# Kernel tuning notes

Measured on AMD Instinct MI355X. Metric: run time of the kernel, lower is better.

The kernel has to match this reference:

```python
import jax, jax.numpy as jnp
import numpy as np

N_NODES = 100000
N_EDGES = 3200000
INPUT_DIM = 128
HIDDEN = 64


def spmm(row, col, vals, x, n):
    # out[i] = sum_{e: row[e]==i} vals[e] * x[col[e]]  -- COO SpMM via gather + segment_sum
    msgs = vals[:, None] * x[col]  # [E, F]
    return jax.ops.segment_sum(msgs, row, num_segments=n)


def setup_inputs() -> dict:
    key = jax.random.key(0)
    ks = jax.random.split(key, 12)
    embeddings = jax.random.normal(ks[0], (N_NODES, INPUT_DIM), dtype=jnp.float32)
    norm_degrees = jax.random.uniform(ks[1], (N_NODES, 1), dtype=jnp.float32)
    seed_mask = (jax.random.uniform(ks[2], (N_NODES, 1)) < 0.05).astype(jnp.float32)
    adj_row = jax.random.randint(ks[3], (N_EDGES,), 0, N_NODES, dtype=jnp.int32)
    adj_col = jax.random.randint(ks[4], (N_EDGES,), 0, N_NODES, dtype=jnp.int32)
    adj_vals = jax.random.uniform(ks[5], (N_EDGES,), dtype=jnp.float32)
    d_in = INPUT_DIM + 2
    # Linear params (torch Linear: y = x @ W.T + b); store W as [in, out]
    W1 = jax.random.normal(ks[6], (d_in, HIDDEN), dtype=jnp.float32) / np.sqrt(d_in)
    b1 = jnp.zeros((HIDDEN,), dtype=jnp.float32)
    W2 = jax.random.normal(ks[7], (HIDDEN, HIDDEN), dtype=jnp.float32) / np.sqrt(HIDDEN)
    b2 = jnp.zeros((HIDDEN,), dtype=jnp.float32)
    W_out = jax.random.normal(ks[8], (HIDDEN, 1), dtype=jnp.float32) / np.sqrt(HIDDEN)
    b_out = jnp.zeros((1,), dtype=jnp.float32)
    return {
        "embeddings": embeddings, "norm_degrees": norm_degrees, "seed_mask": seed_mask,
        "adj_row": adj_row, "adj_col": adj_col, "adj_vals": adj_vals,
        "W1": W1, "b1": b1, "W2": W2, "b2": b2, "W_out": W_out, "b_out": b_out,
    }


def reference(embeddings, norm_degrees, seed_mask, adj_row, adj_col, adj_vals,
              W1, b1, W2, b2, W_out, b_out):
    n = embeddings.shape[0]
    x = jnp.concatenate([embeddings, norm_degrees, seed_mask], axis=1)  # [N, input_dim+2]
    x = x @ W1 + b1                       # conv1
    x = jax.nn.relu(spmm(adj_row, adj_col, adj_vals, x, n))
    x = x @ W2 + b2                       # conv2
    x = jax.nn.relu(spmm(adj_row, adj_col, adj_vals, x, n))
    graph_rep = jnp.sum(x, axis=0)        # [HIDDEN]
    return graph_rep @ W_out + b_out      # [1]
```

## Files before the change

### kernel.cpp

```cpp
#include <hip/hip_runtime.h>
#include <hip/hip_bf16.h>

#define HID 64
#define IN_EMB 128
#define IN_DIM 130
#define ROWS_PER_BKT 512
#define LOG_RPB 9
#define MAX_BKT 256
#define PART_CHUNK 8192
#define SLOT_E 18432
#define ASTR 168
#define BSTR 72
#define ECAP 1024

typedef __hip_bfloat16 bf16;
typedef __attribute__((ext_vector_type(8))) short bf16x8;
typedef __attribute__((ext_vector_type(4))) float fx4;
typedef __attribute__((ext_vector_type(2))) float fx2;

__device__ __forceinline__ short f2bfs(float f) {
  __hip_bfloat16 h = __float2bfloat16(f);
  return *(reinterpret_cast<short*>(&h));
}
__device__ __forceinline__ int pk_fp8x4(float a, float b, float c, float d) {
  int v = __builtin_amdgcn_cvt_pk_fp8_f32(a, b, 0, false);
  v = __builtin_amdgcn_cvt_pk_fp8_f32(c, d, v, true);
  return v;
}
__device__ __forceinline__ unsigned char f2fp8(float x) {
  return (unsigned char)(__builtin_amdgcn_cvt_pk_fp8_f32(x, x, 0, false) & 0xFF);
}

__global__ __launch_bounds__(1024) void bscan_kernel(const int* __restrict__ bcnt,
                                                     int* __restrict__ bstart,
                                                     int* __restrict__ row_ptr,
                                                     int n, int nbkt) {
  __shared__ int s[1024];
  const int t = threadIdx.x;
  const int v = (t < nbkt) ? bcnt[t] : 0;
  s[t] = v;
  __syncthreads();
  for (int off = 1; off < 1024; off <<= 1) {
    int u = (t >= off) ? s[t - off] : 0;
    __syncthreads();
    s[t] += u;
    __syncthreads();
  }
  if (t < nbkt) bstart[t] = s[t] - v;
  if (t == 0) { bstart[nbkt] = s[1023]; row_ptr[n] = s[1023]; }
}

__global__ __launch_bounds__(512) void partition_kernel(
    const int* __restrict__ row, const int* __restrict__ col,
    const float* __restrict__ vals, int* __restrict__ bcur,
    int2* __restrict__ tmp, int nE) {
  __shared__ int h[MAX_BKT];
  __shared__ int cur[MAX_BKT];
  const int t = threadIdx.x;
  const int base = blockIdx.x * PART_CHUNK;
  for (int i = t; i < MAX_BKT; i += 512) h[i] = 0;
  __syncthreads();
  for (int kk = t; kk < PART_CHUNK / 4; kk += 512) {
    int e0 = base + kk * 4;
    if (e0 + 3 < nE) {
      int4 r4 = ((const int4*)row)[(base >> 2) + kk];
      atomicAdd(&h[r4.x >> LOG_RPB], 1);
      atomicAdd(&h[r4.y >> LOG_RPB], 1);
      atomicAdd(&h[r4.z >> LOG_RPB], 1);
      atomicAdd(&h[r4.w >> LOG_RPB], 1);
    } else {
      for (int j = 0; j < 4; ++j) {
        int e = e0 + j;
        if (e < nE) atomicAdd(&h[row[e] >> LOG_RPB], 1);
      }
    }
  }
  __syncthreads();
  for (int b = t; b < MAX_BKT; b += 512)
    if (h[b] > 0) cur[b] = b * SLOT_E + atomicAdd(&bcur[b], h[b]);
  __syncthreads();
  for (int kk = t; kk < PART_CHUNK / 4; kk += 512) {
    int e0 = base + kk * 4;
    if (e0 + 3 < nE) {
      int4 r4 = ((const int4*)row)[(base >> 2) + kk];
      int4 c4 = ((const int4*)col)[(base >> 2) + kk];
      float4 v4 = ((const float4*)vals)[(base >> 2) + kk];
      int rr[4] = {r4.x, r4.y, r4.z, r4.w};
      int cc[4] = {c4.x, c4.y, c4.z, c4.w};
      float vv[4] = {v4.x, v4.y, v4.z, v4.w};
#pragma unroll
      for (int j = 0; j < 4; ++j) {
        int b = rr[j] >> LOG_RPB;
        int p = atomicAdd(&cur[b], 1);
        if (p - b * SLOT_E < SLOT_E)
          tmp[p] = make_int2(cc[j] | ((rr[j] & (ROWS_PER_BKT - 1)) << 20),
                             __float_as_int(vv[j]));
      }
    } else {
      for (int j = 0; j < 4; ++j) {
        int e = e0 + j;
        if (e < nE) {
          int r = row[e];
          int b = r >> LOG_RPB;
          int p = atomicAdd(&cur[b], 1);
          if (p - b * SLOT_E < SLOT_E)
            tmp[p] = make_int2(col[e] | ((r & (ROWS_PER_BKT - 1)) << 20),
                               __float_as_int(vals[e]));
        }
      }
    }
  }
}

__global__ __launch_bounds__(512) void bucket_sort_kernel(
    const int* __restrict__ bstart, const int2* __restrict__ tmp,
    int2* __restrict__ ce, int* __restrict__ row_ptr, int n) {
  __shared__ int rcnt[ROWS_PER_BKT];
  __shared__ int rpos[ROWS_PER_BKT];
  __shared__ int sc[ROWS_PER_BKT];
  const int t = threadIdx.x;
  const int b = blockIdx.x;
  const int start = bstart[b];
  const int len   = bstart[b + 1] - start;
  const int2* ts = tmp + (size_t)b * SLOT_E;
  rcnt[t] = 0;
  __syncthreads();
  const int* keys = (const int*)ts;
  for (int i = t; i < len; i += 512)
    atomicAdd(&rcnt[((unsigned)keys[2 * i]) >> 20], 1);
  __syncthreads();
  sc[t] = rcnt[t];
  __syncthreads();
  for (int off = 1; off < ROWS_PER_BKT; off <<= 1) {
    int u = (t >= off) ? sc[t - off] : 0;
    __syncthreads();
    sc[t] += u;
    __syncthreads();
  }
  {
    int ex = sc[t] - rcnt[t];
    int gpos = start + ex;
    rpos[t] = gpos;
    int gr = b * ROWS_PER_BKT + t;
    if (gr < n) row_ptr[gr] = gpos;
  }
  __syncthreads();
  for (int i = t; i < len; i += 512) {
    int2 e = ts[i];
    int p = atomicAdd(&rpos[((unsigned)e.x) >> 20], 1);
    ce[p] = make_int2(e.x & 0xFFFFF, e.y);
  }
}

__global__ __launch_bounds__(256) void lin1_kernel(
    const float* __restrict__ emb, const float* __restrict__ deg,
    const float* __restrict__ seed, const float* __restrict__ W1,
    const float* __restrict__ b1, unsigned char* __restrict__ out, int n) {
  __shared__ short sB[64 * ASTR];
  const int t = threadIdx.x;
  const int base = blockIdx.x * 256;

  for (int idx = t; idx < 64 * 160; idx += 256) {
    int k = idx >> 6, nn = idx & 63;
    float v = (k < IN_DIM) ? W1[k * HID + nn] : 0.f;
    sB[nn * ASTR + k] = f2bfs(v);
  }
  __syncthreads();

  const int lane = t & 63, w = t >> 6;
  const int nl = lane & 15, q = lane >> 4;
  const short* pB = &sB[nl * ASTR + q * 8];
  const float bias0 = b1[nl], bias1 = b1[16 + nl],
              bias2 = b1[32 + nl], bias3 = b1[48 + nl];

#pragma unroll
  for (int tile = 0; tile < 4; ++tile) {
    const int g64 = base + tile * 64;
    const int anode = g64 + w * 16 + nl;
    bf16x8 afr[5];
    if (anode < n) {
      const float4* ep = (const float4*)(emb + (size_t)anode * IN_EMB);
#pragma unroll
      for (int kt = 0; kt < 4; ++kt) {
        float4 v0 = ep[q * 2 + kt * 8];
        float4 v1 = ep[q * 2 + 1 + kt * 8];
        bf16x8 a;
        a[0] = f2bfs(v0.x); a[1] = f2bfs(v0.y); a[2] = f2bfs(v0.z); a[3] = f2bfs(v0.w);
        a[4] = f2bfs(v1.x); a[5] = f2bfs(v1.y); a[6] = f2bfs(v1.z); a[7] = f2bfs(v1.w);
        afr[kt] = a;
      }
      bf16x8 a4 = {0, 0, 0, 0, 0, 0, 0, 0};
      if (q == 0) { a4[0] = f2bfs(deg[anode]); a4[1] = f2bfs(seed[anode]); }
      afr[4] = a4;
    } else {
#pragma unroll
      for (int kt = 0; kt < 5; ++kt) afr[kt] = (bf16x8){0, 0, 0, 0, 0, 0, 0, 0};
    }

    fx4 ac0 = {0.f, 0.f, 0.f, 0.f}, ac1 = ac0, ac2 = ac0, ac3 = ac0;
#pragma unroll
    for (int kt = 0; kt < 5; ++kt) {
      bf16x8 b0  = *(const bf16x8*)(pB + kt * 32);
      bf16x8 b1v = *(const bf16x8*)(pB + 16 * ASTR + kt * 32);
      bf16x8 b2v = *(const bf16x8*)(pB + 32 * ASTR + kt * 32);
      bf16x8 b3v = *(const bf16x8*)(pB + 48 * ASTR + kt * 32);
      ac0 = __builtin_amdgcn_mfma_f32_16x16x32_bf16(afr[kt], b0,  ac0, 0, 0, 0);
      ac1 = __builtin_amdgcn_mfma_f32_16x16x32_bf16(afr[kt], b1v, ac1, 0, 0, 0);
      ac2 = __builtin_amdgcn_mfma_f32_16x16x32_bf16(afr[kt], b2v, ac2, 0, 0, 0);
      ac3 = __builtin_amdgcn_mfma_f32_16x16x32_bf16(afr[kt], b3v, ac3, 0, 0, 0);
    }
#pragma unroll
    for (int r = 0; r < 4; ++r) {
      int node = g64 + w * 16 + q * 4 + r;
      if (node < n) {
        unsigned char* o = out + ((size_t)node << 6);
        o[nl]      = f2fp8(ac0[r] + bias0);
        o[16 + nl] = f2fp8(ac1[r] + bias1);
        o[32 + nl] = f2fp8(ac2[r] + bias2);
        o[48 + nl] = f2fp8(ac3[r] + bias3);
      }
    }
  }
}

#define GLD(ev, u)                                                            \
  const uint2 u = *(const uint2*)(xp + (((size_t)(unsigned)(ev)) << 6) + 8 * fl);
#define GMAD(ev, u)                                                           \
  {                                                                           \
    const float v = __int_as_float((int)((ev) >> 32));                        \
    const fx2 v2 = {v, v};                                                    \
    a0 += v2 * __builtin_amdgcn_cvt_pk_f32_fp8(u.x, false);                   \
    a1 += v2 * __builtin_amdgcn_cvt_pk_f32_fp8(u.x, true);                    \
    a2 += v2 * __builtin_amdgcn_cvt_pk_f32_fp8(u.y, false);                   \
    a3 += v2 * __builtin_amdgcn_cvt_pk_f32_fp8(u.y, true);                    \
  }
#define GMAD_P(ev, u, ok)                                                     \
  {                                                                           \
    const float v = (ok) ? __int_as_float((int)((ev) >> 32)) : 0.f;           \
    const fx2 v2 = {v, v};                                                    \
    a0 += v2 * __builtin_amdgcn_cvt_pk_f32_fp8(u.x, false);                   \
    a1 += v2 * __builtin_amdgcn_cvt_pk_f32_fp8(u.x, true);                    \
    a2 += v2 * __builtin_amdgcn_cvt_pk_f32_fp8(u.y, false);                   \
    a3 += v2 * __builtin_amdgcn_cvt_pk_f32_fp8(u.y, true);                    \
  }

#define SPMM_STAGE_EDGES                                                      \
  const unsigned long long* cep = (const unsigned long long*)ce;              \
  const int r0blk = blockIdx.x * 4;                                           \
  const int bstartE = row_ptr[r0blk];                                         \
  const int bendE = row_ptr[(r0blk + 4 < n) ? (r0blk + 4) : n];               \
  const int cnt = min(bendE - bstartE, ECAP);                                 \
  for (int ii = threadIdx.x; ii < cnt; ii += 256)                             \
    eb[ii] = __builtin_nontemporal_load(cep + bstartE + ii);                  \
  __syncthreads();

#define SPMM_GATHER_BODY                                                      \
  const int i0r = row_ptr[r];                                                 \
  const int endr = row_ptr[r + 1];                                            \
  int li = i0r - bstartE;                                                     \
  const int lend = endr - bstartE;                                            \
  if (lend <= cnt) {                                                          \
    for (; li + 32 <= lend; li += 32) {                                       \
      unsigned long long e0 = eb[li + sub];                                   \
      unsigned long long e1 = eb[li + 8 + sub];                               \
      unsigned long long e2 = eb[li + 16 + sub];                              \
      unsigned long long e3 = eb[li + 24 + sub];                              \
      GLD(e0, u0); GLD(e1, u1); GLD(e2, u2); GLD(e3, u3);                     \
      GMAD(e0, u0); GMAD(e1, u1); GMAD(e2, u2); GMAD(e3, u3);                 \
    }                                                                         \
    if (li < lend) {                                                          \
      const int last = lend - 1;                                              \
      int i0 = li + sub;        bool k0 = i0 < lend;                          \
      int i1 = li + 8 + sub;    bool k1 = i1 < lend;                          \
      int i2 = li + 16 + sub;   bool k2 = i2 < lend;                          \
      int i3 = li + 24 + sub;   bool k3 = i3 < lend;                          \
      unsigned long long e0 = eb[k0 ? i0 : last];                             \
      unsigned long long e1 = eb[k1 ? i1 : last];                             \
      unsigned long long e2 = eb[k2 ? i2 : last];                             \
      unsigned long long e3 = eb[k3 ? i3 : last];                             \
      GLD(e0, u0); GLD(e1, u1); GLD(e2, u2); GLD(e3, u3);                     \
      GMAD_P(e0, u0, k0); GMAD_P(e1, u1, k1);                                 \
      GMAD_P(e2, u2, k2); GMAD_P(e3, u3, k3);                                 \
    }                                                                         \
  } else {                                                                    \
    int i = i0r;                                                              \
    for (; i + 32 <= endr; i += 32) {                                         \
      unsigned long long e0 = __builtin_nontemporal_load(cep + i + sub);      \
      unsigned long long e1 = __builtin_nontemporal_load(cep + i + 8 + sub);  \
      unsigned long long e2 = __builtin_nontemporal_load(cep + i + 16 + sub); \
      unsigned long long e3 = __builtin_nontemporal_load(cep + i + 24 + sub); \
      GLD(e0, u0); GLD(e1, u1); GLD(e2, u2); GLD(e3, u3);                     \
      GMAD(e0, u0); GMAD(e1, u1); GMAD(e2, u2); GMAD(e3, u3);                 \
    }                                                                         \
    if (i < endr) {                                                           \
      const int last = endr - 1;                                              \
      int i0 = i + sub;        bool k0 = i0 < endr;                           \
      int i1 = i + 8 + sub;    bool k1 = i1 < endr;                           \
      int i2 = i + 16 + sub;   bool k2 = i2 < endr;                           \
      int i3 = i + 24 + sub;   bool k3 = i3 < endr;                           \
      unsigned long long e0 = cep[k0 ? i0 : last];                            \
      unsigned long long e1 = cep[k1 ? i1 : last];                            \
      unsigned long long e2 = cep[k2 ? i2 : last];                            \
      unsigned long long e3 = cep[k3 ? i3 : last];                            \
      GLD(e0, u0); GLD(e1, u1); GLD(e2, u2); GLD(e3, u3);                     \
      GMAD_P(e0, u0, k0); GMAD_P(e1, u1, k1);                                 \
      GMAD_P(e2, u2, k2); GMAD_P(e3, u3, k3);                                 \
    }                                                                         \
  }                                                                           \
                      \
  _Pragma("unroll")                                                           \
  for (int off = 8; off <= 32; off <<= 1) {                                   \
    a0.x += __shfl_xor(a0.x, off); a0.y += __shfl_xor(a0.y, off);             \
    a1.x += __shfl_xor(a1.x, off); a1.y += __shfl_xor(a1.y, off);             \
    a2.x += __shfl_xor(a2.x, off); a2.y += __shfl_xor(a2.y, off);             \
    a3.x += __shfl_xor(a3.x, off); a3.y += __shfl_xor(a3.y, off);             \
  }

__global__ __launch_bounds__(256) void spmm_csr_kernel(
    const int* __restrict__ row_ptr, const int2* __restrict__ ce,
    const unsigned char* __restrict__ x, unsigned char* __restrict__ y, int n) {
  __shared__ unsigned long long eb[ECAP];
  const int lane = threadIdx.x & 63;
  const int sub = lane >> 3;
  const int fl  = lane & 7;
  const int r = blockIdx.x * 4 + (threadIdx.x >> 6);
  const unsigned char* xp = x;
  SPMM_STAGE_EDGES
  if (r < n) {
    fx2 a0 = {0.f, 0.f}, a1 = a0, a2 = a0, a3 = a0;
    SPMM_GATHER_BODY
    if (sub == 0) {
      int lo = pk_fp8x4(fmaxf(a0.x, 0.f), fmaxf(a0.y, 0.f),
                        fmaxf(a1.x, 0.f), fmaxf(a1.y, 0.f));
      int hi = pk_fp8x4(fmaxf(a2.x, 0.f), fmaxf(a2.y, 0.f),
                        fmaxf(a3.x, 0.f), fmaxf(a3.y, 0.f));
      *(int2*)(y + ((size_t)r << 6) + 8 * fl) = make_int2(lo, hi);
    }
  }
}

__global__ __launch_bounds__(256) void lin2_kernel(
    const unsigned char* __restrict__ yin, const float* __restrict__ W2,
    const float* __restrict__ b2, unsigned char* __restrict__ xout, int n) {
  __shared__ short sB[64 * BSTR];
  const int t = threadIdx.x;
  const int base = blockIdx.x * 256;
  for (int idx = t; idx < 64 * 64; idx += 256) {
    int k = idx >> 6, nn = idx & 63;
    sB[nn * BSTR + k] = f2bfs(W2[k * HID + nn]);
  }
  __syncthreads();

  const int lane = t & 63, w = t >> 6;
  const int nl = lane & 15, q = lane >> 4;
  const short* pB = &sB[nl * BSTR + q * 8];
  const float bias0 = b2[nl], bias1 = b2[16 + nl],
              bias2 = b2[32 + nl], bias3 = b2[48 + nl];

#pragma unroll
  for (int tile = 0; tile < 4; ++tile) {
    const int g64 = base + tile * 64;
    const int anode = g64 + w * 16 + nl;
    const unsigned char* xg = yin + (((size_t)anode) << 6) + q * 8;
    fx4 ac0 = {0.f, 0.f, 0.f, 0.f}, ac1 = ac0, ac2 = ac0, ac3 = ac0;
#pragma unroll
    for (int kt = 0; kt < 2; ++kt) {
      uint2 u8 = (anode < n) ? *(const uint2*)(xg + kt * 32) : make_uint2(0u, 0u);
      fx2 f0 = __builtin_amdgcn_cvt_pk_f32_fp8(u8.x, false);
      fx2 f1 = __builtin_amdgcn_cvt_pk_f32_fp8(u8.x, true);
      fx2 f2 = __builtin_amdgcn_cvt_pk_f32_fp8(u8.y, false);
      fx2 f3 = __builtin_amdgcn_cvt_pk_f32_fp8(u8.y, true);
      bf16x8 a;
      a[0] = f2bfs(f0.x); a[1] = f2bfs(f0.y); a[2] = f2bfs(f1.x); a[3] = f2bfs(f1.y);
      a[4] = f2bfs(f2.x); a[5] = f2bfs(f2.y); a[6] = f2bfs(f3.x); a[7] = f2bfs(f3.y);
      bf16x8 b0  = *(const bf16x8*)(pB + kt * 32);
      bf16x8 b1v = *(const bf16x8*)(pB + 16 * BSTR + kt * 32);
      bf16x8 b2v = *(const bf16x8*)(pB + 32 * BSTR + kt * 32);
      bf16x8 b3v = *(const bf16x8*)(pB + 48 * BSTR + kt * 32);
      ac0 = __builtin_amdgcn_mfma_f32_16x16x32_bf16(a, b0,  ac0, 0, 0, 0);
      ac1 = __builtin_amdgcn_mfma_f32_16x16x32_bf16(a, b1v, ac1, 0, 0, 0);
      ac2 = __builtin_amdgcn_mfma_f32_16x16x32_bf16(a, b2v, ac2, 0, 0, 0);
      ac3 = __builtin_amdgcn_mfma_f32_16x16x32_bf16(a, b3v, ac3, 0, 0, 0);
    }
#pragma unroll
    for (int r = 0; r < 4; ++r) {
      int node = g64 + w * 16 + q * 4 + r;
      if (node < n) {
        unsigned char* o = xout + ((size_t)node << 6);
        o[nl]      = f2fp8(ac0[r] + bias0);
        o[16 + nl] = f2fp8(ac1[r] + bias1);
        o[32 + nl] = f2fp8(ac2[r] + bias2);
        o[48 + nl] = f2fp8(ac3[r] + bias3);
      }
    }
  }
}

__global__ __launch_bounds__(256) void spmm2_fused_kernel(
    const int* __restrict__ row_ptr, const int2* __restrict__ ce,
    const unsigned char* __restrict__ x, const float* __restrict__ Wout,
    float* __restrict__ partials, int n) {
  __shared__ unsigned long long eb[ECAP];
  const int lane = threadIdx.x & 63;
  const int sub = lane >> 3;
  const int fl  = lane & 7;
  const int g = threadIdx.x >> 6;
  const int r = blockIdx.x * 4 + g;
  const unsigned char* xp = x;
  SPMM_STAGE_EDGES
  float wpart = 0.f;
  if (r < n) {
    fx2 a0 = {0.f, 0.f}, a1 = a0, a2 = a0, a3 = a0;
    SPMM_GATHER_BODY
    if (sub == 0) {
      const float4 wv0 = ((const float4*)Wout)[2 * fl];
      const float4 wv1 = ((const float4*)Wout)[2 * fl + 1];
      wpart = fmaxf(a0.x, 0.f) * wv0.x + fmaxf(a0.y, 0.f) * wv0.y
            + fmaxf(a1.x, 0.f) * wv0.z + fmaxf(a1.y, 0.f) * wv0.w
            + fmaxf(a2.x, 0.f) * wv1.x + fmaxf(a2.y, 0.f) * wv1.y
            + fmaxf(a3.x, 0.f) * wv1.z + fmaxf(a3.y, 0.f) * wv1.w;
    }
  }
  for (int off = 32; off; off >>= 1) wpart += __shfl_down(wpart, off, 64);
  __shared__ float part[4];
  if (lane == 0) part[g] = wpart;
  __syncthreads();
  if (threadIdx.x == 0)
    partials[blockIdx.x] = part[0] + part[1] + part[2] + part[3];
}

__global__ __launch_bounds__(1024) void reduce_kernel(
    const float* __restrict__ partials, const float* __restrict__ bout,
    float* __restrict__ out, int m) {
  const int t = threadIdx.x;
  float s = 0.f;
  const int m4 = m >> 2;
  for (int i = t; i < m4; i += 1024) {
    float4 v = ((const float4*)partials)[i];
    s += v.x + v.y + v.z + v.w;
  }
  if (t < (m & 3)) s += partials[(m & ~3) + t];
  for (int off = 32; off; off >>= 1) s += __shfl_down(s, off, 64);
  __shared__ float wsum[16];
  if ((t & 63) == 0) wsum[t >> 6] = s;
  __syncthreads();
  if (t == 0) {
    float tot = bout[0];
    for (int w = 0; w < 16; ++w) tot += wsum[w];
    out[0] = tot;
  }
}

extern "C" void kernel_launch(void* const* d_in, const int* in_sizes, int n_in,
                              void* d_out, int out_size, void* d_ws, size_t ws_size,
                              hipStream_t stream) {
  const float* emb  = (const float*)d_in[0];
  const float* deg  = (const float*)d_in[1];
  const float* seed = (const float*)d_in[2];
  const int*   row  = (const int*)d_in[3];
  const int*   col  = (const int*)d_in[4];
  const float* vals = (const float*)d_in[5];
  const float* W1   = (const float*)d_in[6];
  const float* b1   = (const float*)d_in[7];
  const float* W2   = (const float*)d_in[8];
  const float* b2   = (const float*)d_in[9];
  const float* Wout = (const float*)d_in[10];
  const float* bout = (const float*)d_in[11];
  float* out = (float*)d_out;

  const int n  = in_sizes[0] / IN_EMB;
  const int nE = in_sizes[3];
  const int nbkt = (n + ROWS_PER_BKT - 1) / ROWS_PER_BKT;

  const int lin_blocks  = (n + 255) / 256;
  const int row_blocks  = (n + 3) / 4;
  const int part_blocks = (nE + PART_CHUNK - 1) / PART_CHUNK;

  char* ws = (char*)d_ws;
  int2* ce   = (int2*)ws;  ws += (size_t)nE * sizeof(int2);
  char* tmpb = ws;
  int2* tmp  = (int2*)ws;  ws += (size_t)nbkt * SLOT_E * sizeof(int2);
  unsigned char* xb = (unsigned char*)ws;  ws += ((size_t)n * HID + 255) & ~255ULL;
  int* row_ptr = (int*)ws; ws += ((size_t)(n + 1) * 4 + 255) & ~255ULL;
  int* bcur    = (int*)ws; ws += ((size_t)nbkt * 4 + 255) & ~255ULL;
  int* bstart  = (int*)ws; ws += ((size_t)(nbkt + 1) * 4 + 255) & ~255ULL;
  float* partials = (float*)ws;
  unsigned char* xa = (unsigned char*)tmpb;
  unsigned char* ya = (unsigned char*)(tmpb + (8u << 20));

  hipMemsetAsync(bcur, 0, (size_t)nbkt * sizeof(int), stream);
  partition_kernel<<<part_blocks, 512, 0, stream>>>(row, col, vals, bcur, tmp, nE);
  bscan_kernel<<<1, 1024, 0, stream>>>(bcur, bstart, row_ptr, n, nbkt);
  bucket_sort_kernel<<<nbkt, 512, 0, stream>>>(bstart, tmp, ce, row_ptr, n);

  lin1_kernel<<<lin_blocks, 256, 0, stream>>>(emb, deg, seed, W1, b1, xa, n);
  spmm_csr_kernel<<<row_blocks, 256, 0, stream>>>(row_ptr, ce, xa, ya, n);
  lin2_kernel<<<lin_blocks, 256, 0, stream>>>(ya, W2, b2, xb, n);
  spmm2_fused_kernel<<<row_blocks, 256, 0, stream>>>(row_ptr, ce, xb, Wout, partials, n);
  reduce_kernel<<<1, 1024, 0, stream>>>(partials, bout, out, row_blocks);
}
```

Before: 331.5 us.

## Map each SpMM row to 8 lanes instead of a full wavefront

The CSR SpMM kernels now assign one row per group of 8 lanes, 32 rows per 256-thread block, rather than one row per 64-lane wavefront. Each lane walks the row's edges sequentially in steps of 4, which removes the cross-lane shuffle reduction and leaves no lanes idle in the output stage. The shared-memory edge staging buffer is doubled to cover 32 rows' edges. The cost is less memory-level parallelism per row and more lane divergence between rows of different degree, plus higher LDS use per block.

```diff
diff --git a/kernel.cpp b/kernel.cpp
--- a/kernel.cpp
+++ b/kernel.cpp
@@ -11,7 +11,8 @@
 #define SLOT_E 18432
 #define ASTR 168
 #define BSTR 72
-#define ECAP 1024
+#define RPB 32
+#define ECAP 2048
 
 typedef __hip_bfloat16 bf16;
 typedef __attribute__((ext_vector_type(8))) short bf16x8;
@@ -246,9 +247,9 @@
 
 #define SPMM_STAGE_EDGES                                                      \
   const unsigned long long* cep = (const unsigned long long*)ce;              \
-  const int r0blk = blockIdx.x * 4;                                           \
+  const int r0blk = blockIdx.x * RPB;                                         \
   const int bstartE = row_ptr[r0blk];                                         \
-  const int bendE = row_ptr[(r0blk + 4 < n) ? (r0blk + 4) : n];               \
+  const int bendE = row_ptr[(r0blk + RPB < n) ? (r0blk + RPB) : n];           \
   const int cnt = min(bendE - bstartE, ECAP);                                 \
   for (int ii = threadIdx.x; ii < cnt; ii += 256)                             \
     eb[ii] = __builtin_nontemporal_load(cep + bstartE + ii);                  \
@@ -257,85 +258,67 @@
 #define SPMM_GATHER_BODY                                                      \
   const int i0r = row_ptr[r];                                                 \
   const int endr = row_ptr[r + 1];                                            \
-  int li = i0r - bstartE;                                                     \
   const int lend = endr - bstartE;                                            \
   if (lend <= cnt) {                                                          \
-    for (; li + 32 <= lend; li += 32) {                                       \
-      unsigned long long e0 = eb[li + sub];                                   \
-      unsigned long long e1 = eb[li + 8 + sub];                               \
-      unsigned long long e2 = eb[li + 16 + sub];                              \
-      unsigned long long e3 = eb[li + 24 + sub];                              \
+    int i = i0r - bstartE;                                                    \
+    for (; i + 4 <= lend; i += 4) {                                           \
+      unsigned long long e0 = eb[i];                                          \
+      unsigned long long e1 = eb[i + 1];                                      \
+      unsigned long long e2 = eb[i + 2];                                      \
+      unsigned long long e3 = eb[i + 3];                                      \
       GLD(e0, u0); GLD(e1, u1); GLD(e2, u2); GLD(e3, u3);                     \
       GMAD(e0, u0); GMAD(e1, u1); GMAD(e2, u2); GMAD(e3, u3);                 \
     }                                                                         \
-    if (li < lend) {                                                          \
+    if (i < lend) {                                                           \
       const int last = lend - 1;                                              \
-      int i0 = li + sub;        bool k0 = i0 < lend;                          \
-      int i1 = li + 8 + sub;    bool k1 = i1 < lend;                          \
-      int i2 = li + 16 + sub;   bool k2 = i2 < lend;                          \
-      int i3 = li + 24 + sub;   bool k3 = i3 < lend;                          \
-      unsigned long long e0 = eb[k0 ? i0 : last];                             \
-      unsigned long long e1 = eb[k1 ? i1 : last];                             \
-      unsigned long long e2 = eb[k2 ? i2 : last];                             \
-      unsigned long long e3 = eb[k3 ? i3 : last];                             \
+      bool k1 = i + 1 < lend, k2 = i + 2 < lend, k3 = i + 3 < lend;           \
+      unsigned long long e0 = eb[i];                                          \
+      unsigned long long e1 = eb[k1 ? i + 1 : last];                          \
+      unsigned long long e2 = eb[k2 ? i + 2 : last];                          \
+      unsigned long long e3 = eb[k3 ? i + 3 : last];                          \
       GLD(e0, u0); GLD(e1, u1); GLD(e2, u2); GLD(e3, u3);                     \
-      GMAD_P(e0, u0, k0); GMAD_P(e1, u1, k1);                                 \
+      GMAD(e0, u0); GMAD_P(e1, u1, k1);                                       \
       GMAD_P(e2, u2, k2); GMAD_P(e3, u3, k3);                                 \
     }                                                                         \
   } else {                                                                    \
     int i = i0r;                                                              \
-    for (; i + 32 <= endr; i += 32) {                                         \
-      unsigned long long e0 = __builtin_nontemporal_load(cep + i + sub);      \
-      unsigned long long e1 = __builtin_nontemporal_load(cep + i + 8 + sub);  \
-      unsigned long long e2 = __builtin_nontemporal_load(cep + i + 16 + sub); \
-      unsigned long long e3 = __builtin_nontemporal_load(cep + i + 24 + sub); \
+    for (; i + 4 <= endr; i += 4) {                                           \
+      unsigned long long e0 = __builtin_nontemporal_load(cep + i);            \
+      unsigned long long e1 = __builtin_nontemporal_load(cep + i + 1);        \
+      unsigned long long e2 = __builtin_nontemporal_load(cep + i + 2);        \
+      unsigned long long e3 = __builtin_nontemporal_load(cep + i + 3);        \
       GLD(e0, u0); GLD(e1, u1); GLD(e2, u2); GLD(e3, u3);                     \
       GMAD(e0, u0); GMAD(e1, u1); GMAD(e2, u2); GMAD(e3, u3);                 \
     }                                                                         \
     if (i < endr) {                                                           \
       const int last = endr - 1;                                              \
-      int i0 = i + sub;        bool k0 = i0 < endr;                           \
-      int i1 = i + 8 + sub;    bool k1 = i1 < endr;                           \
-      int i2 = i + 16 + sub;   bool k2 = i2 < endr;                           \
-      int i3 = i + 24 + sub;   bool k3 = i3 < endr;                           \
-      unsigned long long e0 = cep[k0 ? i0 : last];                            \
-      unsigned long long e1 = cep[k1 ? i1 : last];                            \
-      unsigned long long e2 = cep[k2 ? i2 : last];                            \
-      unsigned long long e3 = cep[k3 ? i3 : last];                            \
+      bool k1 = i + 1 < endr, k2 = i + 2 < endr, k3 = i + 3 < endr;           \
+      unsigned long long e0 = cep[i];                                         \
+      unsigned long long e1 = cep[k1 ? i + 1 : last];                         \
+      unsigned long long e2 = cep[k2 ? i + 2 : last];                         \
+      unsigned long long e3 = cep[k3 ? i + 3 : last];                         \
       GLD(e0, u0); GLD(e1, u1); GLD(e2, u2); GLD(e3, u3);                     \
-      GMAD_P(e0, u0, k0); GMAD_P(e1, u1, k1);                                 \
+      GMAD(e0, u0); GMAD_P(e1, u1, k1);                                       \
       GMAD_P(e2, u2, k2); GMAD_P(e3, u3, k3);                                 \
     }                                                                         \
-  }                                                                           \
-                      \
-  _Pragma("unroll")                                                           \
-  for (int off = 8; off <= 32; off <<= 1) {                                   \
-    a0.x += __shfl_xor(a0.x, off); a0.y += __shfl_xor(a0.y, off);             \
-    a1.x += __shfl_xor(a1.x, off); a1.y += __shfl_xor(a1.y, off);             \
-    a2.x += __shfl_xor(a2.x, off); a2.y += __shfl_xor(a2.y, off);             \
-    a3.x += __shfl_xor(a3.x, off); a3.y += __shfl_xor(a3.y, off);             \
   }
 
 __global__ __launch_bounds__(256) void spmm_csr_kernel(
     const int* __restrict__ row_ptr, const int2* __restrict__ ce,
     const unsigned char* __restrict__ x, unsigned char* __restrict__ y, int n) {
   __shared__ unsigned long long eb[ECAP];
-  const int lane = threadIdx.x & 63;
-  const int sub = lane >> 3;
-  const int fl  = lane & 7;
-  const int r = blockIdx.x * 4 + (threadIdx.x >> 6);
+  const int fl = threadIdx.x & 7;
+  const int r = blockIdx.x * RPB + (threadIdx.x >> 3);
   const unsigned char* xp = x;
   SPMM_STAGE_EDGES
   if (r < n) {
     fx2 a0 = {0.f, 0.f}, a1 = a0, a2 = a0, a3 = a0;
     SPMM_GATHER_BODY
-    if (sub == 0) {
-      int lo = pk_fp8x4(fmaxf(a0.x, 0.f), fmaxf(a0.y, 0.f),
-                        fmaxf(a1.x, 0.f), fmaxf(a1.y, 0.f));
-      int hi = pk_fp8x4(fmaxf(a2.x, 0.f), fmaxf(a2.y, 0.f),
-                        fmaxf(a3.x, 0.f), fmaxf(a3.y, 0.f));
-      *(int2*)(y + ((size_t)r << 6) + 8 * fl) = make_int2(lo, hi);
-    }
+    int lo = pk_fp8x4(fmaxf(a0.x, 0.f), fmaxf(a0.y, 0.f),
+                      fmaxf(a1.x, 0.f), fmaxf(a1.y, 0.f));
+    int hi = pk_fp8x4(fmaxf(a2.x, 0.f), fmaxf(a2.y, 0.f),
+                      fmaxf(a3.x, 0.f), fmaxf(a3.y, 0.f));
+    *(int2*)(y + ((size_t)r << 6) + 8 * fl) = make_int2(lo, hi);
   }
 }
 
@@ -401,29 +384,25 @@
     const unsigned char* __restrict__ x, const float* __restrict__ Wout,
     float* __restrict__ partials, int n) {
   __shared__ unsigned long long eb[ECAP];
-  const int lane = threadIdx.x & 63;
-  const int sub = lane >> 3;
-  const int fl  = lane & 7;
-  const int g = threadIdx.x >> 6;
-  const int r = blockIdx.x * 4 + g;
+  const int fl = threadIdx.x & 7;
+  const int r = blockIdx.x * RPB + (threadIdx.x >> 3);
   const unsigned char* xp = x;
   SPMM_STAGE_EDGES
   float wpart = 0.f;
   if (r < n) {
     fx2 a0 = {0.f, 0.f}, a1 = a0, a2 = a0, a3 = a0;
     SPMM_GATHER_BODY
-    if (sub == 0) {
-      const float4 wv0 = ((const float4*)Wout)[2 * fl];
-      const float4 wv1 = ((const float4*)Wout)[2 * fl + 1];
-      wpart = fmaxf(a0.x, 0.f) * wv0.x + fmaxf(a0.y, 0.f) * wv0.y
-            + fmaxf(a1.x, 0.f) * wv0.z + fmaxf(a1.y, 0.f) * wv0.w
-            + fmaxf(a2.x, 0.f) * wv1.x + fmaxf(a2.y, 0.f) * wv1.y
-            + fmaxf(a3.x, 0.f) * wv1.z + fmaxf(a3.y, 0.f) * wv1.w;
-    }
+    const float4 wv0 = ((const float4*)Wout)[2 * fl];
+    const float4 wv1 = ((const float4*)Wout)[2 * fl + 1];
+    wpart = fmaxf(a0.x, 0.f) * wv0.x + fmaxf(a0.y, 0.f) * wv0.y
+          + fmaxf(a1.x, 0.f) * wv0.z + fmaxf(a1.y, 0.f) * wv0.w
+          + fmaxf(a2.x, 0.f) * wv1.x + fmaxf(a2.y, 0.f) * wv1.y
+          + fmaxf(a3.x, 0.f) * wv1.z + fmaxf(a3.y, 0.f) * wv1.w;
   }
   for (int off = 32; off; off >>= 1) wpart += __shfl_down(wpart, off, 64);
   __shared__ float part[4];
-  if (lane == 0) part[g] = wpart;
+  const int lane = threadIdx.x & 63;
+  if (lane == 0) part[threadIdx.x >> 6] = wpart;
   __syncthreads();
   if (threadIdx.x == 0)
     partials[blockIdx.x] = part[0] + part[1] + part[2] + part[3];
@@ -473,7 +452,7 @@
   const int nbkt = (n + ROWS_PER_BKT - 1) / ROWS_PER_BKT;
 
   const int lin_blocks  = (n + 255) / 256;
-  const int row_blocks  = (n + 3) / 4;
+  const int row_blocks  = (n + RPB - 1) / RPB;
   const int part_blocks = (nE + PART_CHUNK - 1) / PART_CHUNK;
 
   char* ws = (char*)d_ws;
```

New measurement: 297.2 us. 1.12x faster.
